# Performance work log

Hardware: AMD Instinct MI355X
Metric: run time of the kernel (lower is better)

Reference implementation:

```python
import jax, jax.numpy as jnp
import numpy as np

DIM = 2048; S = 2048; B = 2; H = 16
Q_LORA = 1536; KV_LORA = 512
NOPE = 128; ROPE = 64; VHD = 128
QK_HD = NOPE + ROPE  # 192


def _linear_params(key, out_dim, in_dim):
    k1, k2 = jax.random.split(key)
    w = jax.random.normal(k1, (out_dim, in_dim), jnp.float32) * 0.02
    b = jax.random.normal(k2, (out_dim,), jnp.float32) * 0.02
    return w, b


def setup_inputs() -> dict:
    key = jax.random.key(0)
    ks = jax.random.split(key, 8)
    x = jax.random.normal(ks[0], (B, S, DIM), jnp.float32)
    # RoPE tables (interleaved convention, half-dim = ROPE//2)
    inv_freq = 1.0 / (10000.0 ** (jnp.arange(ROPE // 2, dtype=jnp.float32) / (ROPE // 2)))
    ang = jnp.arange(S, dtype=jnp.float32)[:, None] * inv_freq[None, :]  # [S, 32]
    freqs_cos = jnp.cos(ang)
    freqs_sin = jnp.sin(ang)
    Wq_down_w, Wq_down_b = _linear_params(ks[1], Q_LORA, DIM)
    q_norm_w = jnp.ones((Q_LORA,), jnp.float32)
    Wq_up_w, Wq_up_b = _linear_params(ks[2], H * QK_HD, Q_LORA)
    Wkv_down_w, Wkv_down_b = _linear_params(ks[3], KV_LORA + ROPE, DIM)
    kv_norm_w = jnp.ones((KV_LORA,), jnp.float32)
    Wkv_up_w, Wkv_up_b = _linear_params(ks[4], H * (NOPE + VHD), KV_LORA)
    Wo_w, Wo_b = _linear_params(ks[5], DIM, H * VHD)
    return dict(x=x, freqs_cos=freqs_cos, freqs_sin=freqs_sin,
                Wq_down_w=Wq_down_w, Wq_down_b=Wq_down_b, q_norm_w=q_norm_w,
                Wq_up_w=Wq_up_w, Wq_up_b=Wq_up_b,
                Wkv_down_w=Wkv_down_w, Wkv_down_b=Wkv_down_b, kv_norm_w=kv_norm_w,
                Wkv_up_w=Wkv_up_w, Wkv_up_b=Wkv_up_b, Wo_w=Wo_w, Wo_b=Wo_b)


def _rmsnorm(x, w):
    eps = jnp.finfo(x.dtype).eps
    var = jnp.mean(jnp.square(x), axis=-1, keepdims=True)
    return x * jax.lax.rsqrt(var + eps) * w


def _rope(x, cos, sin):
    # x: [B, S, H, D] with consecutive (real, imag) pairs; cos/sin: [S, D//2]
    xr = x[..., 0::2]
    xi = x[..., 1::2]
    c = cos[None, :, None, :]
    s = sin[None, :, None, :]
    yr = xr * c - xi * s
    yi = xr * s + xi * c
    return jnp.stack([yr, yi], axis=-1).reshape(x.shape)


def reference(x, freqs_cos, freqs_sin, Wq_down_w, Wq_down_b, q_norm_w,
              Wq_up_w, Wq_up_b, Wkv_down_w, Wkv_down_b, kv_norm_w,
              Wkv_up_w, Wkv_up_b, Wo_w, Wo_b):
    Bx, Sx, _ = x.shape
    # Q path: down-proj -> RMSNorm -> up-proj
    q_lat = _rmsnorm(x @ Wq_down_w.T + Wq_down_b, q_norm_w)
    Q = (q_lat @ Wq_up_w.T + Wq_up_b).reshape(Bx, Sx, H, QK_HD)
    Q_nope, Q_rope = Q[..., :NOPE], Q[..., NOPE:]
    Q_rope = _rope(Q_rope, freqs_cos, freqs_sin)
    Q = jnp.concatenate([Q_nope, Q_rope], axis=-1)
    # KV path
    kv = x @ Wkv_down_w.T + Wkv_down_b
    kv_lat, k_rope = kv[..., :KV_LORA], kv[..., KV_LORA:]
    kv_lat = _rmsnorm(kv_lat, kv_norm_w)
    k_rope = _rope(k_rope[:, :, None, :], freqs_cos, freqs_sin)  # [B,S,1,ROPE]
    knv = (kv_lat @ Wkv_up_w.T + Wkv_up_b).reshape(Bx, Sx, H, NOPE + VHD)
    K_nope, V = knv[..., :NOPE], knv[..., NOPE:]
    K = jnp.concatenate([K_nope, jnp.broadcast_to(k_rope, (Bx, Sx, H, ROPE))], axis=-1)
    # causal SDPA, scale = 1/sqrt(qk_head_dim)
    scale = QK_HD ** -0.5
    scores = jnp.einsum('bqhd,bkhd->bhqk', Q, K) * scale
    causal = jnp.tril(jnp.ones((Sx, Sx), bool))
    scores = jnp.where(causal[None, None], scores, jnp.finfo(scores.dtype).min)
    attn = jax.nn.softmax(scores, axis=-1)
    out = jnp.einsum('bhqk,bkhd->bqhd', attn, V).reshape(Bx, Sx, H * VHD)
    return out @ Wo_w.T + Wo_b
```

## Files before the change

kernel.cpp:

```cpp
#include <hip/hip_runtime.h>

typedef unsigned short u16;
typedef short s16x8 __attribute__((ext_vector_type(8)));
typedef short s16x4 __attribute__((ext_vector_type(4)));
typedef float f32x4 __attribute__((ext_vector_type(4)));

#define SEQ   2048
#define BATCH 2
#define NHEAD 16

__device__ __forceinline__ float b2f(u16 u) {
    unsigned x = ((unsigned)u) << 16;
    return __builtin_bit_cast(float, x);
}
__device__ __forceinline__ u16 f2b(float f) {
    unsigned x = __builtin_bit_cast(unsigned, f);
    unsigned r = (x + 0x7fffu + ((x >> 16) & 1u)) >> 16;
    return (u16)r;
}
__device__ __forceinline__ s16x8 comb(s16x4 lo, s16x4 hi) {
    return __builtin_shufflevector(lo, hi, 0, 1, 2, 3, 4, 5, 6, 7);
}
__device__ __forceinline__ void gload16(const void* g, void* l) {
    __builtin_amdgcn_global_load_lds(
        (const __attribute__((address_space(1))) void*)g,
        (__attribute__((address_space(3))) void*)l, 16, 0, 0);
}

__global__ __launch_bounds__(256) void cvt4_k(
    const float* __restrict__ x, const float* __restrict__ wqd,
    const float* __restrict__ wkvd, const float* __restrict__ wqu,
    u16* __restrict__ xb, u16* __restrict__ wqdb,
    u16* __restrict__ wkvdb, u16* __restrict__ wqub)
{
    const int total = 4358144;
    int i = blockIdx.x * 256 + threadIdx.x;
    const int stride = gridDim.x * 256;
    for (; i < total; i += stride) {
        const float4* src; ushort4* dst; int off;
        if (i < 2097152)      { src = (const float4*)x;    dst = (ushort4*)xb;    off = i; }
        else if (i < 2883584) { src = (const float4*)wqd;  dst = (ushort4*)wqdb;  off = i - 2097152; }
        else if (i < 3178496) { src = (const float4*)wkvd; dst = (ushort4*)wkvdb; off = i - 2883584; }
        else                  { src = (const float4*)wqu;  dst = (ushort4*)wqub;  off = i - 3178496; }
        float4 v = src[off];
        ushort4 o = { f2b(v.x), f2b(v.y), f2b(v.z), f2b(v.w) };
        dst[off] = o;
    }
}

__global__ __launch_bounds__(256) void cvt_bf16_k(
    const float* __restrict__ in, u16* __restrict__ out, int n4)
{
    int i = blockIdx.x * 256 + threadIdx.x;
    const int stride = gridDim.x * 256;
    for (; i < n4; i += stride) {
        float4 v = ((const float4*)in)[i];
        ushort4 o = { f2b(v.x), f2b(v.y), f2b(v.z), f2b(v.w) };
        ((ushort4*)out)[i] = o;
    }
}

template <int OUT_BF16>
__global__ __launch_bounds__(256) void gemm_bf_k(
    const u16* __restrict__ A, const u16* __restrict__ W,
    const float* __restrict__ bias, void* __restrict__ Cout,
    int M, int N, int K, int lda)
{
    __shared__ u16 lsA[128 * 64];
    __shared__ u16 lsB[128 * 64];
    const int tid  = threadIdx.x;
    const int lane = tid & 63;
    const int w    = tid >> 6;
    const int wm   = w >> 1, wn = w & 1;
    const int row0 = blockIdx.y * 128;
    const int col0 = blockIdx.x * 128;
    const int lr8  = lane >> 3;
    const int lc8  = (lane & 7) * 8;

    f32x4 acc[4][4];
#pragma unroll
    for (int i = 0; i < 4; i++)
#pragma unroll
        for (int j = 0; j < 4; j++) acc[i][j] = (f32x4){0.f, 0.f, 0.f, 0.f};

    for (int kt = 0; kt < K; kt += 64) {
#pragma unroll
        for (int t = 0; t < 4; t++) {
            const int r = w * 32 + t * 8;
            gload16(A + (size_t)(row0 + r + lr8) * lda + kt + lc8, &lsA[r * 64]);
            int rw = col0 + r + lr8; if (rw >= N) rw = N - 1;
            gload16(W + (size_t)rw * K + kt + lc8, &lsB[r * 64]);
        }
        __syncthreads();
#pragma unroll
        for (int ks = 0; ks < 2; ks++) {
            const int ko = ks * 32 + (lane >> 4) * 8;
            s16x8 af[4], bfr[4];
#pragma unroll
            for (int i = 0; i < 4; i++) {
                af[i]  = *(const s16x8*)&lsA[(wm * 64 + i * 16 + (lane & 15)) * 64 + ko];
                bfr[i] = *(const s16x8*)&lsB[(wn * 64 + i * 16 + (lane & 15)) * 64 + ko];
            }
#pragma unroll
            for (int mf = 0; mf < 4; mf++)
#pragma unroll
                for (int nf = 0; nf < 4; nf++)
                    acc[mf][nf] = __builtin_amdgcn_mfma_f32_16x16x32_bf16(
                        af[mf], bfr[nf], acc[mf][nf], 0, 0, 0);
        }
        __syncthreads();
    }

    const int rb = row0 + wm * 64 + ((lane >> 4) << 2);
    const int cb = col0 + wn * 64 + (lane & 15);
#pragma unroll
    for (int nf = 0; nf < 4; nf++) {
        const int col = cb + nf * 16;
        if (col < N) {
            const float bv = bias[col];
#pragma unroll
            for (int mf = 0; mf < 4; mf++)
#pragma unroll
                for (int r = 0; r < 4; r++) {
                    const int row = rb + mf * 16 + r;
                    float v = acc[mf][nf][r] + bv;
                    if (OUT_BF16) ((u16*)Cout)[(size_t)row * N + col] = f2b(v);
                    else          ((float*)Cout)[(size_t)row * N + col] = v;
                }
        }
    }
}

__global__ __launch_bounds__(256) void gemm_down_k(
    const u16* __restrict__ A, const u16* __restrict__ W0,
    const u16* __restrict__ W1, const float* __restrict__ b0,
    const float* __restrict__ b1, u16* __restrict__ C0, u16* __restrict__ C1)
{
    __shared__ u16 lsA[128 * 64];
    __shared__ u16 lsB[128 * 64];
    const int tid  = threadIdx.x;
    const int lane = tid & 63;
    const int w    = tid >> 6;
    const int wm   = w >> 1, wn = w & 1;
    const int row0 = blockIdx.y * 128;
    const int col0 = blockIdx.x * 128;
    const int lr8  = lane >> 3;
    const int lc8  = (lane & 7) * 8;
    const bool in1 = (col0 >= 1536);
    const u16* Wm  = in1 ? W1 : W0;
    const int wbase = in1 ? col0 - 1536 : col0;
    const int wmax  = in1 ? 575 : 1535;

    f32x4 acc[4][4];
#pragma unroll
    for (int i = 0; i < 4; i++)
#pragma unroll
        for (int j = 0; j < 4; j++) acc[i][j] = (f32x4){0.f, 0.f, 0.f, 0.f};

    for (int kt = 0; kt < 2048; kt += 64) {
#pragma unroll
        for (int t = 0; t < 4; t++) {
            const int r = w * 32 + t * 8;
            gload16(A + (size_t)(row0 + r + lr8) * 2048 + kt + lc8, &lsA[r * 64]);
            int rw = wbase + r + lr8; if (rw > wmax) rw = wmax;
            gload16(Wm + (size_t)rw * 2048 + kt + lc8, &lsB[r * 64]);
        }
        __syncthreads();
#pragma unroll
        for (int ks = 0; ks < 2; ks++) {
            const int ko = ks * 32 + (lane >> 4) * 8;
            s16x8 af[4], bfr[4];
#pragma unroll
            for (int i = 0; i < 4; i++) {
                af[i]  = *(const s16x8*)&lsA[(wm * 64 + i * 16 + (lane & 15)) * 64 + ko];
                bfr[i] = *(const s16x8*)&lsB[(wn * 64 + i * 16 + (lane & 15)) * 64 + ko];
            }
#pragma unroll
            for (int mf = 0; mf < 4; mf++)
#pragma unroll
                for (int nf = 0; nf < 4; nf++)
                    acc[mf][nf] = __builtin_amdgcn_mfma_f32_16x16x32_bf16(
                        af[mf], bfr[nf], acc[mf][nf], 0, 0, 0);
        }
        __syncthreads();
    }

    const int rb = row0 + wm * 64 + ((lane >> 4) << 2);
    const int cb = col0 + wn * 64 + (lane & 15);
#pragma unroll
    for (int nf = 0; nf < 4; nf++) {
        const int col = cb + nf * 16;
        if (col < 2112) {
            const bool c1 = (col >= 1536);
            const float bv = c1 ? b1[col - 1536] : b0[col];
#pragma unroll
            for (int mf = 0; mf < 4; mf++)
#pragma unroll
                for (int r = 0; r < 4; r++) {
                    const int row = rb + mf * 16 + r;
                    float v = acc[mf][nf][r] + bv;
                    if (c1) C1[(size_t)row * 576 + col - 1536] = f2b(v);
                    else    C0[(size_t)row * 1536 + col] = f2b(v);
                }
        }
    }
}

__global__ __launch_bounds__(256) void norm_rope_k(
    u16* __restrict__ qlat, u16* __restrict__ kvb,
    const float* __restrict__ qnw, const float* __restrict__ kvnw,
    const float* __restrict__ fc, const float* __restrict__ fs,
    u16* __restrict__ krope)
{
    const int bid = blockIdx.x;
    const int row = bid & 4095;
    const bool isq = bid < 4096;
    u16* xr = isq ? qlat + (size_t)row * 1536 : kvb + (size_t)row * 576;
    const int cols = isq ? 1536 : 512;
    const float* wv = isq ? qnw : kvnw;

    if (!isq && threadIdx.x < 32) {
        const int i = threadIdx.x;
        const int s = row & (SEQ - 1);
        const u16* src = kvb + (size_t)row * 576 + 512 + 2 * i;
        const float xr0 = b2f(src[0]), xi0 = b2f(src[1]);
        const float c = fc[s * 32 + i], sn = fs[s * 32 + i];
        ushort2 o;
        o.x = f2b(xr0 * c - xi0 * sn);
        o.y = f2b(xr0 * sn + xi0 * c);
        *((ushort2*)(krope + (size_t)row * 64) + i) = o;
    }

    float ss = 0.f;
    for (int c = threadIdx.x; c < cols; c += 256) { float v = b2f(xr[c]); ss += v * v; }
#pragma unroll
    for (int off = 32; off; off >>= 1) ss += __shfl_xor(ss, off);
    __shared__ float red[4];
    if ((threadIdx.x & 63) == 0) red[threadIdx.x >> 6] = ss;
    __syncthreads();
    const float tot = red[0] + red[1] + red[2] + red[3];
    const float inv = rsqrtf(tot / (float)cols + 1.1920929e-7f);
    for (int c = threadIdx.x; c < cols; c += 256)
        xr[c] = f2b(b2f(xr[c]) * inv * wv[c]);
}

__global__ __launch_bounds__(256) void rope_q_k(
    u16* __restrict__ qb, const float* __restrict__ fc, const float* __restrict__ fs)
{
    const int idx = blockIdx.x * 256 + threadIdx.x;
    const int i = idx & 31;
    const int h = (idx >> 5) & 15;
    const int row = idx >> 9;
    const int s = row & (SEQ - 1);
    ushort2* p = (ushort2*)(qb + (size_t)row * 3072 + h * 192 + 128) + i;
    ushort2 v = *p;
    const float xr = b2f(v.x), xi = b2f(v.y);
    const float c = fc[s * 32 + i], sn = fs[s * 32 + i];
    ushort2 o;
    o.x = f2b(xr * c - xi * sn);
    o.y = f2b(xr * sn + xi * c);
    *p = o;
}

__global__ __launch_bounds__(256, 2) void attn_k(
    const u16* __restrict__ Q, const u16* __restrict__ KNV,
    const u16* __restrict__ KR, u16* __restrict__ O)
{
    __shared__ u16 k_lds[64][200];
    __shared__ u16 v_t[128][68];

    const int tid  = threadIdx.x;
    const int lane = tid & 63;
    const int w    = tid >> 6;
    const int lr   = lane & 15;
    const int lq   = lane >> 4;

    const int bid = blockIdx.x;
    const int qt  = (bid < 256) ? (15 - (bid >> 5)) : ((bid - 256) >> 5);
    const int bh  = bid & 31;
    const int h   = bh & 15;
    const int b   = bh >> 4;
    const int q0  = qt * 128;
    const int bS  = b * SEQ;

    s16x8 qf[2][6];
#pragma unroll
    for (int mb = 0; mb < 2; mb++) {
        const u16* qp = Q + (size_t)(bS + q0 + w * 32 + mb * 16 + lr) * 3072
                        + h * 192 + (lq << 2);
#pragma unroll
        for (int kc = 0; kc < 6; kc++)
            qf[mb][kc] = comb(*(const s16x4*)(qp + kc * 32),
                              *(const s16x4*)(qp + kc * 32 + 16));
    }

    f32x4 o_acc[2][8];
#pragma unroll
    for (int mb = 0; mb < 2; mb++)
#pragma unroll
        for (int d = 0; d < 8; d++) o_acc[mb][d] = (f32x4){0.f, 0.f, 0.f, 0.f};
    float m_run[2] = { -1e30f, -1e30f };
    float l_run[2] = { 0.f, 0.f };

    const float scale = 0.07216878364870323f;
    const int ntiles = (q0 + 128) / 64;

    s16x8 kr[6], vr[4];
    const int kkey = tid >> 2;
    const int ka   = tid & 3;

    {
        const u16* kn  = KNV + (size_t)(bS + kkey) * 4096 + h * 256;
        const u16* krp = KR + (size_t)(bS + kkey) * 64;
#pragma unroll
        for (int i = 0; i < 6; i++) {
            const int col = ka * 48 + i * 8;
            kr[i] = *(const s16x8*)(col < 128 ? kn + col : krp + (col - 128));
        }
#pragma unroll
        for (int i = 0; i < 4; i++) {
            const int idx = tid + i * 256;
            vr[i] = *(const s16x8*)(KNV + (size_t)(bS + (idx >> 4)) * 4096
                                    + h * 256 + 128 + (idx & 15) * 8);
        }
    }

    for (int t = 0; t < ntiles; t++) {
#pragma unroll
        for (int i = 0; i < 6; i++)
            *(s16x8*)&k_lds[kkey][ka * 48 + i * 8] = kr[i];
#pragma unroll
        for (int i = 0; i < 4; i++) {
            const int idx = tid + i * 256;
            const int key = idx >> 4, d0 = (idx & 15) * 8;
            const int xw = (d0 >> 4) << 2;
#pragma unroll
            for (int e = 0; e < 8; e++) v_t[d0 + e][key ^ xw] = (u16)vr[i][e];
        }
        __syncthreads();

        if (t + 1 < ntiles) {
            const int nk = (t + 1) * 64;
            const u16* kn  = KNV + (size_t)(bS + nk + kkey) * 4096 + h * 256;
            const u16* krp = KR + (size_t)(bS + nk + kkey) * 64;
#pragma unroll
            for (int i = 0; i < 6; i++) {
                const int col = ka * 48 + i * 8;
                kr[i] = *(const s16x8*)(col < 128 ? kn + col : krp + (col - 128));
            }
#pragma unroll
            for (int i = 0; i < 4; i++) {
                const int idx = tid + i * 256;
                vr[i] = *(const s16x8*)(KNV + (size_t)(bS + nk + (idx >> 4)) * 4096
                                        + h * 256 + 128 + (idx & 15) * 8);
            }
        }

        const int kt0 = t * 64;

        f32x4 sa[2][4];
#pragma unroll
        for (int mb = 0; mb < 2; mb++)
#pragma unroll
            for (int f = 0; f < 4; f++) sa[mb][f] = (f32x4){0.f, 0.f, 0.f, 0.f};
#pragma unroll
        for (int kc = 0; kc < 6; kc++) {
            const int kb = kc * 32 + (lq << 2);
#pragma unroll
            for (int f = 0; f < 4; f++) {
                s16x8 kf = comb(*(const s16x4*)&k_lds[f * 16 + lr][kb],
                                *(const s16x4*)&k_lds[f * 16 + lr][kb + 16]);
                sa[0][f] = __builtin_amdgcn_mfma_f32_16x16x32_bf16(kf, qf[0][kc], sa[0][f], 0, 0, 0);
                sa[1][f] = __builtin_amdgcn_mfma_f32_16x16x32_bf16(kf, qf[1][kc], sa[1][f], 0, 0, 0);
            }
        }

        s16x8 pb[2][2];
#pragma unroll
        for (int mb = 0; mb < 2; mb++) {
            const int qrow = q0 + w * 32 + mb * 16 + lr;
            const bool need_mask = (kt0 + 63 > qrow);
            float p[4][4];
#pragma unroll
            for (int f = 0; f < 4; f++)
#pragma unroll
                for (int r = 0; r < 4; r++) {
                    float s = sa[mb][f][r] * scale;
                    if (need_mask && (kt0 + f * 16 + lq * 4 + r > qrow)) s = -1e30f;
                    p[f][r] = s;
                }
            float tm = p[0][0];
#pragma unroll
            for (int f = 0; f < 4; f++)
#pragma unroll
                for (int r = 0; r < 4; r++) tm = fmaxf(tm, p[f][r]);
            tm = fmaxf(tm, __shfl_xor(tm, 16));
            tm = fmaxf(tm, __shfl_xor(tm, 32));

            const float mo = m_run[mb];
            const bool keep = __all(tm <= mo + 8.f);
            float corr = 1.f;
            if (!keep) {
                const float nm = fmaxf(mo, tm);
                corr = __expf(mo - nm);
                m_run[mb] = nm;
            }
            const float mb_base = m_run[mb];
#pragma unroll
            for (int f = 0; f < 4; f++)
#pragma unroll
                for (int r = 0; r < 4; r++)
                    p[f][r] = __expf(p[f][r] - mb_base);
            float ps = 0.f;
#pragma unroll
            for (int f = 0; f < 4; f++)
#pragma unroll
                for (int r = 0; r < 4; r++) ps += p[f][r];
            ps += __shfl_xor(ps, 16);
            ps += __shfl_xor(ps, 32);
            l_run[mb] = l_run[mb] * corr + ps;
            if (!keep) {
#pragma unroll
                for (int d = 0; d < 8; d++)
#pragma unroll
                    for (int r = 0; r < 4; r++) o_acc[mb][d][r] *= corr;
            }
#pragma unroll
            for (int hf = 0; hf < 2; hf++) {
                s16x8 v;
#pragma unroll
                for (int j = 0; j < 8; j++)
                    v[j] = (short)f2b(p[hf * 2 + (j >> 2)][j & 3]);
                pb[mb][hf] = v;
            }
        }

#pragma unroll
        for (int hf = 0; hf < 2; hf++) {
            const int pc = hf * 32 + (lq << 2);
#pragma unroll
            for (int df = 0; df < 8; df++) {
                const int row = df * 16 + lr;
                const int xr0 = df << 2;
                s16x8 vf = comb(*(const s16x4*)&v_t[row][pc ^ xr0],
                                *(const s16x4*)&v_t[row][(pc + 16) ^ xr0]);
                o_acc[0][df] = __builtin_amdgcn_mfma_f32_16x16x32_bf16(vf, pb[0][hf], o_acc[0][df], 0, 0, 0);
                o_acc[1][df] = __builtin_amdgcn_mfma_f32_16x16x32_bf16(vf, pb[1][hf], o_acc[1][df], 0, 0, 0);
            }
        }
        __syncthreads();
    }

#pragma unroll
    for (int mb = 0; mb < 2; mb++) {
        const float invl = 1.f / l_run[mb];
        u16* op = O + (size_t)(bS + q0 + w * 32 + mb * 16 + lr) * 2048 + h * 128 + lq * 4;
#pragma unroll
        for (int df = 0; df < 8; df++) {
            ushort4 ov = { f2b(o_acc[mb][df][0] * invl), f2b(o_acc[mb][df][1] * invl),
                           f2b(o_acc[mb][df][2] * invl), f2b(o_acc[mb][df][3] * invl) };
            *(ushort4*)(op + df * 16) = ov;
        }
    }
}

extern "C" void kernel_launch(void* const* d_in, const int* in_sizes, int n_in,
                              void* d_out, int out_size, void* d_ws, size_t ws_size,
                              hipStream_t stream)
{
    const float* x    = (const float*)d_in[0];
    const float* fc   = (const float*)d_in[1];
    const float* fs   = (const float*)d_in[2];
    const float* Wqd  = (const float*)d_in[3];
    const float* bqd  = (const float*)d_in[4];
    const float* qnw  = (const float*)d_in[5];
    const float* Wqu  = (const float*)d_in[6];
    const float* bqu  = (const float*)d_in[7];
    const float* Wkvd = (const float*)d_in[8];
    const float* bkvd = (const float*)d_in[9];
    const float* kvnw = (const float*)d_in[10];
    const float* Wkvu = (const float*)d_in[11];
    const float* bkvu = (const float*)d_in[12];
    const float* Wo   = (const float*)d_in[13];
    const float* bo   = (const float*)d_in[14];

    char* ws = (char*)d_ws;
    u16* kvb     = (u16*)(ws);
    u16* qlat    = (u16*)(ws + 4718592);
    u16* qbuf    = (u16*)(ws + 17301504);
    u16* krope   = (u16*)(ws + 42467328);
    u16* knv     = (u16*)(ws + 42991616);
    u16* attn_o  = (u16*)(ws);
    u16* x_bf    = (u16*)(ws + 17301504);
    u16* wqd_bf  = (u16*)(ws + 42991616);
    u16* wkvd_bf = (u16*)(ws + 49283072);
    u16* wqu_bf  = (u16*)(ws + 51642368);
    u16* wkvu_bf = (u16*)(ws + 4718592);
    u16* wo_bf   = (u16*)(ws + 42991616);

    const int M = BATCH * SEQ;

    cvt4_k<<<2048, 256, 0, stream>>>(x, Wqd, Wkvd, Wqu, x_bf, wqd_bf, wkvd_bf, wqu_bf);
    gemm_down_k<<<dim3(17, 32), 256, 0, stream>>>(x_bf, wqd_bf, wkvd_bf, bqd, bkvd, qlat, kvb);
    norm_rope_k<<<8192, 256, 0, stream>>>(qlat, kvb, qnw, kvnw, fc, fs, krope);
    gemm_bf_k<1><<<dim3(24, 32), 256, 0, stream>>>(qlat, wqu_bf, bqu, qbuf, M, 3072, 1536, 1536);
    rope_q_k<<<(M * 16 * 32) / 256, 256, 0, stream>>>(qbuf, fc, fs);
    cvt_bf16_k<<<1024, 256, 0, stream>>>(Wkvu, wkvu_bf, 2097152 / 4);
    gemm_bf_k<1><<<dim3(32, 32), 256, 0, stream>>>(kvb, wkvu_bf, bkvu, knv, M, 4096, 512, 576);
    attn_k<<<512, 256, 0, stream>>>(qbuf, knv, krope, attn_o);
    cvt_bf16_k<<<1024, 256, 0, stream>>>(Wo, wo_bf, 4194304 / 4);
    gemm_bf_k<0><<<dim3(16, 32), 256, 0, stream>>>(attn_o, wo_bf, bo, (float*)d_out, M, 2048, 2048, 2048);
}
```

Baseline: 403.8 us.

## Fuse Q RoPE and softmax scale into Q up-projection, use exp2 in attention

Adds a dedicated Q up-projection GEMM whose epilogue applies RoPE through lane shuffles and multiplies by scale*log2(e), which removes the separate rope_q_k pass over Q. Attention then drops its per-score scale multiply and uses native exp2. It also packs P to bf16 with v_cvt_pk_bf16_f32 and rotates the element order of the V transpose writes to reduce LDS bank conflicts. Folding the scale into Q before bf16 rounding slightly changes numerics.

```diff
diff --git a/kernel.cpp b/kernel.cpp
--- a/kernel.cpp
+++ b/kernel.cpp
@@ -25,6 +25,11 @@
     __builtin_amdgcn_global_load_lds(
         (const __attribute__((address_space(1))) void*)g,
         (__attribute__((address_space(3))) void*)l, 16, 0, 0);
+}
+__device__ __forceinline__ unsigned cvtpk(float lo, float hi) {
+    unsigned r;
+    asm("v_cvt_pk_bf16_f32 %0, %1, %2" : "=v"(r) : "v"(lo), "v"(hi));
+    return r;
 }
 
 __global__ __launch_bounds__(256) void cvt4_k(
@@ -128,6 +133,83 @@
                     else          ((float*)Cout)[(size_t)row * N + col] = v;
                 }
         }
+    }
+}
+
+__global__ __launch_bounds__(256) void gemm_qup_k(
+    const u16* __restrict__ A, const u16* __restrict__ W,
+    const float* __restrict__ bias, u16* __restrict__ Cout,
+    const float* __restrict__ fc, const float* __restrict__ fs)
+{
+    __shared__ u16 lsA[128 * 64];
+    __shared__ u16 lsB[128 * 64];
+    const int tid  = threadIdx.x;
+    const int lane = tid & 63;
+    const int w    = tid >> 6;
+    const int wm   = w >> 1, wn = w & 1;
+    const int row0 = blockIdx.y * 128;
+    const int col0 = blockIdx.x * 128;
+    const int lr8  = lane >> 3;
+    const int lc8  = (lane & 7) * 8;
+    const float QS = 0.10411754f;
+
+    f32x4 acc[4][4];
+#pragma unroll
+    for (int i = 0; i < 4; i++)
+#pragma unroll
+        for (int j = 0; j < 4; j++) acc[i][j] = (f32x4){0.f, 0.f, 0.f, 0.f};
+
+    for (int kt = 0; kt < 1536; kt += 64) {
+#pragma unroll
+        for (int t = 0; t < 4; t++) {
+            const int r = w * 32 + t * 8;
+            gload16(A + (size_t)(row0 + r + lr8) * 1536 + kt + lc8, &lsA[r * 64]);
+            gload16(W + (size_t)(col0 + r + lr8) * 1536 + kt + lc8, &lsB[r * 64]);
+        }
+        __syncthreads();
+#pragma unroll
+        for (int ks = 0; ks < 2; ks++) {
+            const int ko = ks * 32 + (lane >> 4) * 8;
+            s16x8 af[4], bfr[4];
+#pragma unroll
+            for (int i = 0; i < 4; i++) {
+                af[i]  = *(const s16x8*)&lsA[(wm * 64 + i * 16 + (lane & 15)) * 64 + ko];
+                bfr[i] = *(const s16x8*)&lsB[(wn * 64 + i * 16 + (lane & 15)) * 64 + ko];
+            }
+#pragma unroll
+            for (int mf = 0; mf < 4; mf++)
+#pragma unroll
+                for (int nf = 0; nf < 4; nf++)
+                    acc[mf][nf] = __builtin_amdgcn_mfma_f32_16x16x32_bf16(
+                        af[mf], bfr[nf], acc[mf][nf], 0, 0, 0);
+        }
+        __syncthreads();
+    }
+
+    const int rb = row0 + wm * 64 + ((lane >> 4) << 2);
+    const int cb = col0 + wn * 64 + (lane & 15);
+#pragma unroll
+    for (int nf = 0; nf < 4; nf++) {
+        const int col = cb + nf * 16;
+        const float bv = bias[col];
+        const int colBase = col0 + wn * 64 + nf * 16;
+        const int dh0 = colBase % 192;
+        const bool ropeBlk = (dh0 >= 128);
+        const int ib = (dh0 - 128 + (lane & 15)) >> 1;
+#pragma unroll
+        for (int mf = 0; mf < 4; mf++)
+#pragma unroll
+            for (int r = 0; r < 4; r++) {
+                const int row = rb + mf * 16 + r;
+                float v = acc[mf][nf][r] + bv;
+                if (ropeBlk) {
+                    const float pp = __shfl_xor(v, 1);
+                    const int s = row & (SEQ - 1);
+                    const float c = fc[s * 32 + ib], sn = fs[s * 32 + ib];
+                    v = (lane & 1) ? (v * c + pp * sn) : (v * c - pp * sn);
+                }
+                Cout[(size_t)row * 3072 + col] = f2b(v * QS);
+            }
     }
 }
 
@@ -244,24 +326,6 @@
         xr[c] = f2b(b2f(xr[c]) * inv * wv[c]);
 }
 
-__global__ __launch_bounds__(256) void rope_q_k(
-    u16* __restrict__ qb, const float* __restrict__ fc, const float* __restrict__ fs)
-{
-    const int idx = blockIdx.x * 256 + threadIdx.x;
-    const int i = idx & 31;
-    const int h = (idx >> 5) & 15;
-    const int row = idx >> 9;
-    const int s = row & (SEQ - 1);
-    ushort2* p = (ushort2*)(qb + (size_t)row * 3072 + h * 192 + 128) + i;
-    ushort2 v = *p;
-    const float xr = b2f(v.x), xi = b2f(v.y);
-    const float c = fc[s * 32 + i], sn = fs[s * 32 + i];
-    ushort2 o;
-    o.x = f2b(xr * c - xi * sn);
-    o.y = f2b(xr * sn + xi * c);
-    *p = o;
-}
-
 __global__ __launch_bounds__(256, 2) void attn_k(
     const u16* __restrict__ Q, const u16* __restrict__ KNV,
     const u16* __restrict__ KR, u16* __restrict__ O)
@@ -302,7 +366,6 @@
     float m_run[2] = { -1e30f, -1e30f };
     float l_run[2] = { 0.f, 0.f };
 
-    const float scale = 0.07216878364870323f;
     const int ntiles = (q0 + 128) / 64;
 
     s16x8 kr[6], vr[4];
@@ -335,7 +398,10 @@
             const int key = idx >> 4, d0 = (idx & 15) * 8;
             const int xw = (d0 >> 4) << 2;
 #pragma unroll
-            for (int e = 0; e < 8; e++) v_t[d0 + e][key ^ xw] = (u16)vr[i][e];
+            for (int e = 0; e < 8; e++) {
+                const int ee = (e + tid) & 7;
+                v_t[d0 + ee][key ^ xw] = (u16)vr[i][ee];
+            }
         }
         __syncthreads();
 
@@ -385,7 +451,7 @@
             for (int f = 0; f < 4; f++)
 #pragma unroll
                 for (int r = 0; r < 4; r++) {
-                    float s = sa[mb][f][r] * scale;
+                    float s = sa[mb][f][r];
                     if (need_mask && (kt0 + f * 16 + lq * 4 + r > qrow)) s = -1e30f;
                     p[f][r] = s;
                 }
@@ -402,15 +468,15 @@
             float corr = 1.f;
             if (!keep) {
                 const float nm = fmaxf(mo, tm);
-                corr = __expf(mo - nm);
+                corr = __builtin_amdgcn_exp2f(mo - nm);
                 m_run[mb] = nm;
             }
-            const float mb_base = m_run[mb];
+            const float mbase = m_run[mb];
 #pragma unroll
             for (int f = 0; f < 4; f++)
 #pragma unroll
                 for (int r = 0; r < 4; r++)
-                    p[f][r] = __expf(p[f][r] - mb_base);
+                    p[f][r] = __builtin_amdgcn_exp2f(p[f][r] - mbase);
             float ps = 0.f;
 #pragma unroll
             for (int f = 0; f < 4; f++)
@@ -427,11 +493,12 @@
             }
 #pragma unroll
             for (int hf = 0; hf < 2; hf++) {
-                s16x8 v;
-#pragma unroll
-                for (int j = 0; j < 8; j++)
-                    v[j] = (short)f2b(p[hf * 2 + (j >> 2)][j & 3]);
-                pb[mb][hf] = v;
+                uint4 uu;
+                uu.x = cvtpk(p[hf * 2][0],     p[hf * 2][1]);
+                uu.y = cvtpk(p[hf * 2][2],     p[hf * 2][3]);
+                uu.z = cvtpk(p[hf * 2 + 1][0], p[hf * 2 + 1][1]);
+                uu.w = cvtpk(p[hf * 2 + 1][2], p[hf * 2 + 1][3]);
+                pb[mb][hf] = __builtin_bit_cast(s16x8, uu);
             }
         }
 
@@ -503,8 +570,7 @@
     cvt4_k<<<2048, 256, 0, stream>>>(x, Wqd, Wkvd, Wqu, x_bf, wqd_bf, wkvd_bf, wqu_bf);
     gemm_down_k<<<dim3(17, 32), 256, 0, stream>>>(x_bf, wqd_bf, wkvd_bf, bqd, bkvd, qlat, kvb);
     norm_rope_k<<<8192, 256, 0, stream>>>(qlat, kvb, qnw, kvnw, fc, fs, krope);
-    gemm_bf_k<1><<<dim3(24, 32), 256, 0, stream>>>(qlat, wqu_bf, bqu, qbuf, M, 3072, 1536, 1536);
-    rope_q_k<<<(M * 16 * 32) / 256, 256, 0, stream>>>(qbuf, fc, fs);
+    gemm_qup_k<<<dim3(24, 32), 256, 0, stream>>>(qlat, wqu_bf, bqu, qbuf, fc, fs);
     cvt_bf16_k<<<1024, 256, 0, stream>>>(Wkvu, wkvu_bf, 2097152 / 4);
     gemm_bf_k<1><<<dim3(32, 32), 256, 0, stream>>>(kvb, wkvu_bf, bkvu, knv, M, 4096, 512, 576);
     attn_k<<<512, 256, 0, stream>>>(qbuf, knv, krope, attn_o);
```

After: 469.0 us. 16.1% more time.
